# Performance work log

Hardware: AMD Instinct MI355X
Metric: run time of the kernel (lower is better)

## Reference

```python
import jax, jax.numpy as jnp
import numpy as np

B, S, D = 1, 4096, 1024
H = 16
HD = D // H  # 64
ROPE_THETA = 10000.0
NEG_INF = -1e9


def setup_inputs() -> dict:
    key = jax.random.key(0)
    ks = jax.random.split(key, 6)
    x = jax.random.normal(ks[0], (B, S, D), dtype=jnp.float32)
    # rotary frequencies: freqs_cis = exp(i * t * theta^{-2j/hd}), j in [0, hd/2)
    inv_freq = 1.0 / (ROPE_THETA ** (jnp.arange(0, HD, 2, dtype=jnp.float32) / HD))  # [HD/2]
    angles = jnp.arange(S, dtype=jnp.float32)[:, None] * inv_freq[None, :]  # [S, HD/2]
    freqs_cos = jnp.cos(angles)
    freqs_sin = jnp.sin(angles)
    # causal additive mask [S, S]
    mask = jnp.where(jnp.triu(jnp.ones((S, S), dtype=bool), k=1), NEG_INF, 0.0).astype(jnp.float32)
    scale = 0.02
    wq = jax.random.normal(ks[1], (D, D), dtype=jnp.float32) * scale
    wk = jax.random.normal(ks[2], (D, D), dtype=jnp.float32) * scale
    wv = jax.random.normal(ks[3], (D, D), dtype=jnp.float32) * scale
    wo = jax.random.normal(ks[4], (D, D), dtype=jnp.float32) * scale
    return {"x": x, "freqs_cos": freqs_cos, "freqs_sin": freqs_sin, "mask": mask,
            "wq": wq, "wk": wk, "wv": wv, "wo": wo}


def _apply_rope(t, cos, sin):
    # t: [B, S, H, HD]; cos/sin: [S, HD/2] -> broadcast [1, S, 1, HD/2]
    tr = t.reshape(*t.shape[:-1], HD // 2, 2)
    te, to = tr[..., 0], tr[..., 1]
    c = cos[None, :, None, :]
    s = sin[None, :, None, :]
    # complex multiply (te + i*to) * (c + i*s)
    oe = te * c - to * s
    oo = te * s + to * c
    return jnp.stack([oe, oo], axis=-1).reshape(t.shape)


def reference(x, freqs_cos, freqs_sin, mask, wq, wk, wv, wo):
    b, s, d = x.shape
    q = (x @ wq.T).reshape(b, s, H, HD)
    k = (x @ wk.T).reshape(b, s, H, HD)
    v = (x @ wv.T).reshape(b, s, H, HD)
    q = _apply_rope(q, freqs_cos, freqs_sin)
    k = _apply_rope(k, freqs_cos, freqs_sin)
    # [B, H, S, HD]
    q = q.transpose(0, 2, 1, 3)
    k = k.transpose(0, 2, 1, 3)
    v = v.transpose(0, 2, 1, 3)
    scores = jnp.einsum('bhqd,bhkd->bhqk', q, k) / jnp.sqrt(jnp.float32(HD))
    scores = scores + mask[None, None, :, :]
    probs = jax.nn.softmax(scores.astype(jnp.float32), axis=-1).astype(q.dtype)
    out = jnp.einsum('bhqk,bhkd->bhqd', probs, v)
    out = out.transpose(0, 2, 1, 3).reshape(b, s, d)
    return out @ wo.T
```

## Files before the change

### kernel.cpp

```cpp
#include <hip/hip_runtime.h>
#include <stdint.h>

typedef _Float16 f16;
typedef _Float16 v2h __attribute__((ext_vector_type(2)));
typedef _Float16 v4h __attribute__((ext_vector_type(4)));
typedef _Float16 v8h __attribute__((ext_vector_type(8)));
typedef float    v4f __attribute__((ext_vector_type(4)));

#define SEQ 4096
#define NH  16
#define DM  1024
#define QSCALE 0.18033688011112042f
#define MBASE 8.0f

__device__ __forceinline__ float exp2_(float x) {
#if __has_builtin(__builtin_amdgcn_exp2f)
  return __builtin_amdgcn_exp2f(x);
#else
  return exp2f(x);
#endif
}

__device__ __forceinline__ void gload_lds16(const void* g, void* l) {
  __builtin_amdgcn_global_load_lds((const __attribute__((address_space(1))) void*)g,
                                   (__attribute__((address_space(3))) void*)l,
                                   16, 0, 0);
}

#define NX 4194304
#define NW 1048576
__global__ void convert_kernel(const float* __restrict__ x,
                               const float* __restrict__ wq, const float* __restrict__ wk,
                               const float* __restrict__ wv, const float* __restrict__ wo,
                               f16* __restrict__ xf, f16* __restrict__ W, f16* __restrict__ Wo) {
  size_t e = ((size_t)blockIdx.x * 256 + threadIdx.x) * 4;
  const float* src; f16* dst;
  if (e < (size_t)NX) { src = x + e; dst = xf + e; }
  else {
    size_t j = e - NX; int wi = (int)(j >> 20); size_t off = j & (NW - 1);
    src = (wi == 0 ? wq : wi == 1 ? wk : wi == 2 ? wv : wo) + off;
    dst = (wi < 3 ? W + (size_t)wi * NW : Wo) + off;
  }
  v4f v = *(const v4f*)src;
  v4h o = { (f16)v.x, (f16)v.y, (f16)v.z, (f16)v.w };
  *(v4h*)dst = o;
}

template <typename OUTT>
__global__ __launch_bounds__(256, 2) void gemm_bt_f16(const f16* __restrict__ A,
                                                      const f16* __restrict__ B,
                                                      OUTT* __restrict__ C,
                                                      int M, int N, int K) {
  __shared__ __align__(16) f16 As[128 * 64];
  __shared__ __align__(16) f16 Bs[128 * 64];
  const int t = threadIdx.x;
  const int w = t >> 6, l = t & 63, quad = l >> 4, l15 = l & 15;
  const int wm = w & 1, wn = w >> 1;
  const int m0 = blockIdx.y * 128, n0 = blockIdx.x * 128;

  v4f acc[4][4];
#pragma unroll
  for (int i = 0; i < 4; ++i)
#pragma unroll
    for (int j = 0; j < 4; ++j) acc[i][j] = v4f{0.f, 0.f, 0.f, 0.f};

  const int nkt = K >> 6;
  for (int kt = 0; kt < nkt; ++kt) {
    __syncthreads();
#pragma unroll
    for (int i = 0; i < 4; ++i) {
      int c = i * 256 + t; int r = c >> 3, cc = c & 7; int sc = cc ^ (r & 7);
      gload_lds16(A + (size_t)(m0 + r) * K + kt * 64 + sc * 8, As + c * 8);
      gload_lds16(B + (size_t)(n0 + r) * K + kt * 64 + sc * 8, Bs + c * 8);
    }
    __syncthreads();
#pragma unroll
    for (int ks = 0; ks < 2; ++ks) {
      v8h af[4], bf[4];
#pragma unroll
      for (int i = 0; i < 4; ++i) {
        int ra = wm * 64 + i * 16 + l15;
        af[i] = *(const v8h*)(As + ra * 64 + (((ks * 4 + quad) ^ (ra & 7)) * 8));
        int rb = wn * 64 + i * 16 + l15;
        bf[i] = *(const v8h*)(Bs + rb * 64 + (((ks * 4 + quad) ^ (rb & 7)) * 8));
      }
#pragma unroll
      for (int i = 0; i < 4; ++i)
#pragma unroll
        for (int j = 0; j < 4; ++j)
          acc[i][j] = __builtin_amdgcn_mfma_f32_16x16x32_f16(af[i], bf[j], acc[i][j], 0, 0, 0);
    }
  }
#pragma unroll
  for (int i = 0; i < 4; ++i) {
    int m = m0 + wm * 64 + i * 16 + quad * 4;
#pragma unroll
    for (int j = 0; j < 4; ++j) {
      int n = n0 + wn * 64 + j * 16 + l15;
#pragma unroll
      for (int rg = 0; rg < 4; ++rg)
        C[(size_t)(m + rg) * N + n] = (OUTT)acc[i][j][rg];
    }
  }
}

__global__ void rope_kernel(const f16* __restrict__ qkv, const float* __restrict__ fc,
                            const float* __restrict__ fs, f16* __restrict__ Qh,
                            f16* __restrict__ Kh) {
  int idx = blockIdx.x * 256 + threadIdx.x;
  int s = idx >> 9, r = idx & 511, h = r >> 5, i = r & 31;
  size_t base = (size_t)s * 3072 + h * 64 + 2 * i;
  float qe = (float)qkv[base], qo = (float)qkv[base + 1];
  float ke = (float)qkv[base + 1024], ko = (float)qkv[base + 1025];
  float c = fc[s * 32 + i], sn = fs[s * 32 + i];
  size_t ob = ((size_t)(h * 4096 + s)) * 64 + 2 * i;
  v2h qo2 = { (f16)((qe * c - qo * sn) * QSCALE), (f16)((qe * sn + qo * c) * QSCALE) };
  v2h ko2 = { (f16)(ke * c - ko * sn), (f16)(ke * sn + ko * c) };
  *(v2h*)(Qh + ob) = qo2;
  *(v2h*)(Kh + ob) = ko2;
}

__global__ void vtrans_kernel(const f16* __restrict__ qkv, f16* __restrict__ Vt) {
  __shared__ __align__(16) f16 T[64][72];
  int h = blockIdx.x >> 6, sb = blockIdx.x & 63;
  int t = threadIdx.x, s0 = sb * 64;
#pragma unroll
  for (int i = 0; i < 2; ++i) {
    int r = i * 32 + (t >> 3), c8 = t & 7;
    *(v8h*)(&T[r][c8 * 8]) = *(const v8h*)(qkv + (size_t)(s0 + r) * 3072 + 2048 + h * 64 + c8 * 8);
  }
  __syncthreads();
#pragma unroll
  for (int i = 0; i < 4; ++i) {
    int idx = i * 256 + t;
    int d = idx >> 4;
    int sq = (idx & 15) * 4;
    int g = sq >> 5;
    int s32 = sq & 31;
    int kap = ((s32 >> 2) & 3) * 8 + (s32 >> 4) * 4;
    v4h o = { T[sq + 0][d], T[sq + 1][d], T[sq + 2][d], T[sq + 3][d] };
    *(v4h*)(Vt + (size_t)(h * 64 + d) * 4096 + s0 + g * 32 + kap) = o;
  }
}

__global__ __launch_bounds__(256, 4) void flash_kernel(const f16* __restrict__ Qh,
                                                       const f16* __restrict__ Kh,
                                                       const f16* __restrict__ Vt,
                                                       f16* __restrict__ Opart,
                                                       float* __restrict__ Lpart) {
  __shared__ __align__(16) f16 SM[16384];
  f16* Ks = SM;
  f16* Vs = SM + 8192;
  const int h = blockIdx.y;
  const int sr = 79 - (int)blockIdx.x;
  int qb, sp, nsp;
  if (sr < 8)       { qb = sr; sp = 0; nsp = 1; }
  else if (sr < 24) { int j = sr - 8;  qb = 8  + (j >> 1); sp = j & 1; nsp = 2; }
  else if (sr < 48) { int j = sr - 24; int q3 = j / 3; qb = 16 + q3; sp = j - 3 * q3; nsp = 3; }
  else              { int j = sr - 48; qb = 24 + (j >> 2); sp = j & 3; nsp = 4; }
  const int S = 2 * qb + 2;
  const int lo = (sp * S) / nsp, hi = ((sp + 1) * S) / nsp - 1;

  const int t = threadIdx.x, w = t >> 6, l = t & 63, quad = l >> 4, l15 = l & 15;
  const int q0w = qb * 128 + w * 32;

  v8h qf[2][2];
#pragma unroll
  for (int qt = 0; qt < 2; ++qt)
#pragma unroll
    for (int ks = 0; ks < 2; ++ks)
      qf[qt][ks] = *(const v8h*)(Qh + ((size_t)(h * 4096 + q0w + qt * 16 + l15)) * 64 + ks * 32 + quad * 8);

  v4f av[2][4];
#pragma unroll
  for (int qt = 0; qt < 2; ++qt)
#pragma unroll
    for (int db = 0; db < 4; ++db) av[qt][db] = v4f{0.f, 0.f, 0.f, 0.f};
  float lrun[2] = { 0.f, 0.f };

  const int c0 = t, c1 = 256 + t;
  const int r0 = c0 >> 3, sc0 = (c0 & 7) ^ (r0 & 7);
  const int r1 = c1 >> 3, sc1 = (c1 & 7) ^ (r1 & 7);
  const f16* KhB = Kh + (size_t)h * 4096 * 64;
  const f16* VtB = Vt + (size_t)h * 64 * 4096;

  {
    int koff = lo * 64;
    f16* Kd = Ks + (lo & 1) * 4096;
    f16* Vd = Vs + (lo & 1) * 4096;
    gload_lds16(KhB + (size_t)(koff + r0) * 64 + sc0 * 8, Kd + c0 * 8);
    gload_lds16(KhB + (size_t)(koff + r1) * 64 + sc1 * 8, Kd + c1 * 8);
    gload_lds16(VtB + (size_t)r0 * 4096 + koff + sc0 * 8, Vd + c0 * 8);
    gload_lds16(VtB + (size_t)r1 * 4096 + koff + sc1 * 8, Vd + c1 * 8);
  }

  for (int kb = lo; kb <= hi; ++kb) {
    __syncthreads();
    if (kb < hi) {
      int nb = (kb + 1) & 1;
      int koff = (kb + 1) * 64;
      gload_lds16(KhB + (size_t)(koff + r0) * 64 + sc0 * 8, Ks + nb * 4096 + c0 * 8);
      gload_lds16(KhB + (size_t)(koff + r1) * 64 + sc1 * 8, Ks + nb * 4096 + c1 * 8);
      gload_lds16(VtB + (size_t)r0 * 4096 + koff + sc0 * 8, Vs + nb * 4096 + c0 * 8);
      gload_lds16(VtB + (size_t)r1 * 4096 + koff + sc1 * 8, Vs + nb * 4096 + c1 * 8);
    }
    if (kb * 64 > q0w + 31) continue;
    const f16* Kc = Ks + (kb & 1) * 4096;
    const f16* Vc = Vs + (kb & 1) * 4096;

    v8h kf[4][2];
#pragma unroll
    for (int kt = 0; kt < 4; ++kt)
#pragma unroll
      for (int ks = 0; ks < 2; ++ks) {
        int r = kt * 16 + l15;
        kf[kt][ks] = *(const v8h*)(Kc + r * 64 + (((ks * 4 + quad) ^ (r & 7)) * 8));
      }

#pragma unroll
    for (int qt = 0; qt < 2; ++qt) {
      int qtb = q0w + qt * 16;
      if (kb * 64 > qtb + 15) continue;
      v4f st[4];
#pragma unroll
      for (int kt = 0; kt < 4; ++kt) {
        v4f z = v4f{ -MBASE, -MBASE, -MBASE, -MBASE };
        z = __builtin_amdgcn_mfma_f32_16x16x32_f16(kf[kt][0], qf[qt][0], z, 0, 0, 0);
        st[kt] = __builtin_amdgcn_mfma_f32_16x16x32_f16(kf[kt][1], qf[qt][1], z, 0, 0, 0);
      }
      if (kb * 64 + 63 > qtb) {
        int qg = qtb + l15;
#pragma unroll
        for (int kt = 0; kt < 4; ++kt)
#pragma unroll
          for (int jj = 0; jj < 4; ++jj) {
            int kg = kb * 64 + kt * 16 + quad * 4 + jj;
            if (kg > qg) st[kt][jj] = -1e30f;
          }
      }
      v4h pf[4];
      float rs = 0.f;
#pragma unroll
      for (int kt = 0; kt < 4; ++kt)
#pragma unroll
        for (int jj = 0; jj < 4; ++jj) {
          float p = exp2_(st[kt][jj]);
          rs += p;
          pf[kt][jj] = (f16)p;
        }
      lrun[qt] += rs;
      v8h pg[2];
#pragma unroll
      for (int g = 0; g < 2; ++g) {
        pg[g][0] = pf[2 * g][0]; pg[g][1] = pf[2 * g][1];
        pg[g][2] = pf[2 * g][2]; pg[g][3] = pf[2 * g][3];
        pg[g][4] = pf[2 * g + 1][0]; pg[g][5] = pf[2 * g + 1][1];
        pg[g][6] = pf[2 * g + 1][2]; pg[g][7] = pf[2 * g + 1][3];
      }
#pragma unroll
      for (int db = 0; db < 4; ++db) {
        int r = db * 16 + l15;
#pragma unroll
        for (int g = 0; g < 2; ++g) {
          v8h vf = *(const v8h*)(Vc + r * 64 + (((g * 4 + quad) ^ (r & 7)) * 8));
          av[qt][db] = __builtin_amdgcn_mfma_f32_16x16x32_f16(vf, pg[g], av[qt][db], 0, 0, 0);
        }
      }
    }
  }
  const size_t base = (size_t)(h * 80 + sr);
#pragma unroll
  for (int qt = 0; qt < 2; ++qt) {
    float lr = lrun[qt];
    lr += __shfl_xor(lr, 16);
    lr += __shfl_xor(lr, 32);
    int q = w * 32 + qt * 16 + l15;
    if (quad == 0) Lpart[base * 128 + q] = lr;
#pragma unroll
    for (int db = 0; db < 4; ++db) {
      v4h o = { (f16)av[qt][db][0], (f16)av[qt][db][1],
                (f16)av[qt][db][2], (f16)av[qt][db][3] };
      *(v4h*)(Opart + base * 8192 + (size_t)q * 64 + db * 16 + quad * 4) = o;
    }
  }
}

__global__ void combine_kernel(const f16* __restrict__ Opart, const float* __restrict__ Lpart,
                               f16* __restrict__ attn) {
  int qb = blockIdx.x, h = blockIdx.y;
  int nsp, base;
  if (qb < 8)       { nsp = 1; base = qb; }
  else if (qb < 16) { nsp = 2; base = 8 + 2 * (qb - 8); }
  else if (qb < 24) { nsp = 3; base = 24 + 3 * (qb - 16); }
  else              { nsp = 4; base = 48 + 4 * (qb - 24); }
  int t = threadIdx.x, q = t >> 1, dh = (t & 1) * 32;
  float l = 0.f;
  float o[32];
#pragma unroll
  for (int c = 0; c < 32; ++c) o[c] = 0.f;
  for (int s = 0; s < nsp; ++s) {
    size_t sb = (size_t)(h * 80 + base + s);
    const f16* P = Opart + sb * 8192 + q * 64 + dh;
#pragma unroll
    for (int c = 0; c < 4; ++c) {
      v8h v = *(const v8h*)(P + c * 8);
#pragma unroll
      for (int j = 0; j < 8; ++j) o[c * 8 + j] += (float)v[j];
    }
    l += Lpart[sb * 128 + q];
  }
  float inv = 1.f / l;
#pragma unroll
  for (int c = 0; c < 4; ++c) {
    v8h v;
#pragma unroll
    for (int j = 0; j < 8; ++j) v[j] = (f16)(o[c * 8 + j] * inv);
    *(v8h*)(attn + (size_t)(qb * 128 + q) * 1024 + h * 64 + dh + c * 8) = v;
  }
}

extern "C" void kernel_launch(void* const* d_in, const int* in_sizes, int n_in,
                              void* d_out, int out_size, void* d_ws, size_t ws_size,
                              hipStream_t stream) {
  (void)in_sizes; (void)n_in; (void)out_size; (void)ws_size;
  const float* x  = (const float*)d_in[0];
  const float* fc = (const float*)d_in[1];
  const float* fs = (const float*)d_in[2];
  const float* wq = (const float*)d_in[4];
  const float* wk = (const float*)d_in[5];
  const float* wv = (const float*)d_in[6];
  const float* wo = (const float*)d_in[7];
  float* out = (float*)d_out;
  char* ws = (char*)d_ws;

  f16* xf    = (f16*)(ws);
  f16* W     = (f16*)(ws + 8388608);
  f16* Wo    = (f16*)(ws + 14680064);
  f16* QKV   = (f16*)(ws + 16777216);
  f16* Qh    = (f16*)(ws + 41943040);
  f16* Kh    = (f16*)(ws + 50331648);
  f16* Vt    = (f16*)(ws + 58720256);
  f16* attn  = xf;
  f16* Opart = QKV;
  float* Lpart = (float*)(ws + 16777216 + 20971520);

  convert_kernel<<<dim3(8192), dim3(256), 0, stream>>>(x, wq, wk, wv, wo, xf, W, Wo);
  gemm_bt_f16<f16><<<dim3(24, 32), dim3(256), 0, stream>>>(xf, W, QKV, 4096, 3072, 1024);
  rope_kernel<<<dim3(8192), dim3(256), 0, stream>>>(QKV, fc, fs, Qh, Kh);
  vtrans_kernel<<<dim3(1024), dim3(256), 0, stream>>>(QKV, Vt);
  flash_kernel<<<dim3(80, 16), dim3(256), 0, stream>>>(Qh, Kh, Vt, Opart, Lpart);
  combine_kernel<<<dim3(32, 16), dim3(256), 0, stream>>>(Opart, Lpart, attn);
  gemm_bt_f16<float><<<dim3(8, 32), dim3(256), 0, stream>>>(attn, Wo, out, 4096, 1024, 1024);
}
```

Measured before the change: 258.5 us.

## Fuse RoPE into QKV GEMM epilogue, retile output GEMM, reorder flash grid

Applies RoPE and the Q scaling directly in the QKV GEMM epilogue. It uses a lane shuffle to fetch the paired even/odd element and writes Q and K straight into the head-major layout, which removes the separate rope kernel and the round trip of Q and K through global memory. V is written to a smaller temporary buffer before the transpose. The output projection gets its own kernel with 128x64 tiles and a 3-block occupancy hint, which doubles the block count for better CU fill. The flash grid is flattened so heads vary fastest, and the P fragment packing is simplified. In exchange, the epilogue stores are scattered 2-byte writes with extra fc/fs loads per element.

```diff
diff --git a/kernel.cpp b/kernel.cpp
--- a/kernel.cpp
+++ b/kernel.cpp
@@ -46,17 +46,21 @@
   *(v4h*)dst = o;
 }
 
-template <typename OUTT>
-__global__ __launch_bounds__(256, 2) void gemm_bt_f16(const f16* __restrict__ A,
-                                                      const f16* __restrict__ B,
-                                                      OUTT* __restrict__ C,
-                                                      int M, int N, int K) {
+__global__ __launch_bounds__(256, 2) void gemm_qkv_kernel(const f16* __restrict__ A,
+                                                          const f16* __restrict__ B,
+                                                          const float* __restrict__ fc,
+                                                          const float* __restrict__ fs,
+                                                          f16* __restrict__ Qh,
+                                                          f16* __restrict__ Kh,
+                                                          f16* __restrict__ Vtmp) {
+  const int K = 1024;
   __shared__ __align__(16) f16 As[128 * 64];
   __shared__ __align__(16) f16 Bs[128 * 64];
   const int t = threadIdx.x;
   const int w = t >> 6, l = t & 63, quad = l >> 4, l15 = l & 15;
   const int wm = w & 1, wn = w >> 1;
-  const int m0 = blockIdx.y * 128, n0 = blockIdx.x * 128;
+  const int bx = blockIdx.x;
+  const int m0 = blockIdx.y * 128, n0 = bx * 128;
 
   v4f acc[4][4];
 #pragma unroll
@@ -64,8 +68,7 @@
 #pragma unroll
     for (int j = 0; j < 4; ++j) acc[i][j] = v4f{0.f, 0.f, 0.f, 0.f};
 
-  const int nkt = K >> 6;
-  for (int kt = 0; kt < nkt; ++kt) {
+  for (int kt = 0; kt < 16; ++kt) {
     __syncthreads();
 #pragma unroll
     for (int i = 0; i < 4; ++i) {
@@ -91,43 +94,52 @@
           acc[i][j] = __builtin_amdgcn_mfma_f32_16x16x32_f16(af[i], bf[j], acc[i][j], 0, 0, 0);
     }
   }
-#pragma unroll
-  for (int i = 0; i < 4; ++i) {
-    int m = m0 + wm * 64 + i * 16 + quad * 4;
+  const int mat = bx >> 3;
+  if (mat < 2) {
+    f16* dst = (mat == 0) ? Qh : Kh;
+    const int hh = (bx & 7) * 2 + wn;
 #pragma unroll
     for (int j = 0; j < 4; ++j) {
-      int n = n0 + wn * 64 + j * 16 + l15;
-#pragma unroll
-      for (int rg = 0; rg < 4; ++rg)
-        C[(size_t)(m + rg) * N + n] = (OUTT)acc[i][j][rg];
-    }
-  }
-}
-
-__global__ void rope_kernel(const f16* __restrict__ qkv, const float* __restrict__ fc,
-                            const float* __restrict__ fs, f16* __restrict__ Qh,
-                            f16* __restrict__ Kh) {
-  int idx = blockIdx.x * 256 + threadIdx.x;
-  int s = idx >> 9, r = idx & 511, h = r >> 5, i = r & 31;
-  size_t base = (size_t)s * 3072 + h * 64 + 2 * i;
-  float qe = (float)qkv[base], qo = (float)qkv[base + 1];
-  float ke = (float)qkv[base + 1024], ko = (float)qkv[base + 1025];
-  float c = fc[s * 32 + i], sn = fs[s * 32 + i];
-  size_t ob = ((size_t)(h * 4096 + s)) * 64 + 2 * i;
-  v2h qo2 = { (f16)((qe * c - qo * sn) * QSCALE), (f16)((qe * sn + qo * c) * QSCALE) };
-  v2h ko2 = { (f16)(ke * c - ko * sn), (f16)(ke * sn + ko * c) };
-  *(v2h*)(Qh + ob) = qo2;
-  *(v2h*)(Kh + ob) = ko2;
-}
-
-__global__ void vtrans_kernel(const f16* __restrict__ qkv, f16* __restrict__ Vt) {
+      const int d = j * 16 + l15;
+      const int i2 = d >> 1;
+      const float sgnmul = (l15 & 1) ? 1.f : -1.f;
+#pragma unroll
+      for (int i = 0; i < 4; ++i) {
+#pragma unroll
+        for (int rg = 0; rg < 4; ++rg) {
+          float own = acc[i][j][rg];
+          float par = __shfl_xor(own, 1);
+          int m = m0 + wm * 64 + i * 16 + quad * 4 + rg;
+          float c = fc[m * 32 + i2], sn = fs[m * 32 + i2];
+          if (mat == 0) { c *= QSCALE; sn *= QSCALE; }
+          float out = own * c + par * (sn * sgnmul);
+          dst[((size_t)(hh * 4096 + m)) * 64 + d] = (f16)out;
+        }
+      }
+    }
+  } else {
+#pragma unroll
+    for (int i = 0; i < 4; ++i) {
+      int m = m0 + wm * 64 + i * 16 + quad * 4;
+#pragma unroll
+      for (int j = 0; j < 4; ++j) {
+        int nf = (bx - 16) * 128 + wn * 64 + j * 16 + l15;
+#pragma unroll
+        for (int rg = 0; rg < 4; ++rg)
+          Vtmp[(size_t)(m + rg) * 1024 + nf] = (f16)acc[i][j][rg];
+      }
+    }
+  }
+}
+
+__global__ void vtrans_kernel(const f16* __restrict__ Vtmp, f16* __restrict__ Vt) {
   __shared__ __align__(16) f16 T[64][72];
   int h = blockIdx.x >> 6, sb = blockIdx.x & 63;
   int t = threadIdx.x, s0 = sb * 64;
 #pragma unroll
   for (int i = 0; i < 2; ++i) {
     int r = i * 32 + (t >> 3), c8 = t & 7;
-    *(v8h*)(&T[r][c8 * 8]) = *(const v8h*)(qkv + (size_t)(s0 + r) * 3072 + 2048 + h * 64 + c8 * 8);
+    *(v8h*)(&T[r][c8 * 8]) = *(const v8h*)(Vtmp + (size_t)(s0 + r) * 1024 + h * 64 + c8 * 8);
   }
   __syncthreads();
 #pragma unroll
@@ -151,8 +163,8 @@
   __shared__ __align__(16) f16 SM[16384];
   f16* Ks = SM;
   f16* Vs = SM + 8192;
-  const int h = blockIdx.y;
-  const int sr = 79 - (int)blockIdx.x;
+  const int h = blockIdx.x & 15;
+  const int sr = 79 - ((int)blockIdx.x >> 4);
   int qb, sp, nsp;
   if (sr < 8)       { qb = sr; sp = 0; nsp = 1; }
   else if (sr < 24) { int j = sr - 8;  qb = 8  + (j >> 1); sp = j & 1; nsp = 2; }
@@ -238,7 +250,7 @@
             if (kg > qg) st[kt][jj] = -1e30f;
           }
       }
-      v4h pf[4];
+      v8h pg[2];
       float rs = 0.f;
 #pragma unroll
       for (int kt = 0; kt < 4; ++kt)
@@ -246,17 +258,9 @@
         for (int jj = 0; jj < 4; ++jj) {
           float p = exp2_(st[kt][jj]);
           rs += p;
-          pf[kt][jj] = (f16)p;
+          pg[kt >> 1][(kt & 1) * 4 + jj] = (f16)p;
         }
       lrun[qt] += rs;
-      v8h pg[2];
-#pragma unroll
-      for (int g = 0; g < 2; ++g) {
-        pg[g][0] = pf[2 * g][0]; pg[g][1] = pf[2 * g][1];
-        pg[g][2] = pf[2 * g][2]; pg[g][3] = pf[2 * g][3];
-        pg[g][4] = pf[2 * g + 1][0]; pg[g][5] = pf[2 * g + 1][1];
-        pg[g][6] = pf[2 * g + 1][2]; pg[g][7] = pf[2 * g + 1][3];
-      }
 #pragma unroll
       for (int db = 0; db < 4; ++db) {
         int r = db * 16 + l15;
@@ -316,6 +320,69 @@
 #pragma unroll
     for (int j = 0; j < 8; ++j) v[j] = (f16)(o[c * 8 + j] * inv);
     *(v8h*)(attn + (size_t)(qb * 128 + q) * 1024 + h * 64 + dh + c * 8) = v;
+  }
+}
+
+__global__ __launch_bounds__(256, 3) void gemm_out_kernel(const f16* __restrict__ A,
+                                                          const f16* __restrict__ B,
+                                                          float* __restrict__ C) {
+  const int K = 1024, N = 1024;
+  __shared__ __align__(16) f16 As[128 * 64];
+  __shared__ __align__(16) f16 Bs[64 * 64];
+  const int t = threadIdx.x;
+  const int w = t >> 6, l = t & 63, quad = l >> 4, l15 = l & 15;
+  const int wm = w & 1, wn = w >> 1;
+  const int m0 = blockIdx.y * 128, n0 = blockIdx.x * 64;
+
+  v4f acc[4][2];
+#pragma unroll
+  for (int i = 0; i < 4; ++i)
+#pragma unroll
+    for (int j = 0; j < 2; ++j) acc[i][j] = v4f{0.f, 0.f, 0.f, 0.f};
+
+  for (int kt = 0; kt < 16; ++kt) {
+    __syncthreads();
+#pragma unroll
+    for (int i = 0; i < 4; ++i) {
+      int c = i * 256 + t; int r = c >> 3, cc = c & 7; int sc = cc ^ (r & 7);
+      gload_lds16(A + (size_t)(m0 + r) * K + kt * 64 + sc * 8, As + c * 8);
+    }
+#pragma unroll
+    for (int i = 0; i < 2; ++i) {
+      int c = i * 256 + t; int r = c >> 3, cc = c & 7; int sc = cc ^ (r & 7);
+      gload_lds16(B + (size_t)(n0 + r) * K + kt * 64 + sc * 8, Bs + c * 8);
+    }
+    __syncthreads();
+#pragma unroll
+    for (int ks = 0; ks < 2; ++ks) {
+      v8h af[4], bf[2];
+#pragma unroll
+      for (int i = 0; i < 4; ++i) {
+        int ra = wm * 64 + i * 16 + l15;
+        af[i] = *(const v8h*)(As + ra * 64 + (((ks * 4 + quad) ^ (ra & 7)) * 8));
+      }
+#pragma unroll
+      for (int j = 0; j < 2; ++j) {
+        int rb = wn * 32 + j * 16 + l15;
+        bf[j] = *(const v8h*)(Bs + rb * 64 + (((ks * 4 + quad) ^ (rb & 7)) * 8));
+      }
+#pragma unroll
+      for (int i = 0; i < 4; ++i)
+#pragma unroll
+        for (int j = 0; j < 2; ++j)
+          acc[i][j] = __builtin_amdgcn_mfma_f32_16x16x32_f16(af[i], bf[j], acc[i][j], 0, 0, 0);
+    }
+  }
+#pragma unroll
+  for (int i = 0; i < 4; ++i) {
+    int m = m0 + wm * 64 + i * 16 + quad * 4;
+#pragma unroll
+    for (int j = 0; j < 2; ++j) {
+      int n = n0 + wn * 32 + j * 16 + l15;
+#pragma unroll
+      for (int rg = 0; rg < 4; ++rg)
+        C[(size_t)(m + rg) * N + n] = acc[i][j][rg];
+    }
   }
 }
 
@@ -336,19 +403,18 @@
   f16* xf    = (f16*)(ws);
   f16* W     = (f16*)(ws + 8388608);
   f16* Wo    = (f16*)(ws + 14680064);
-  f16* QKV   = (f16*)(ws + 16777216);
+  f16* Vtmp  = (f16*)(ws + 16777216);
   f16* Qh    = (f16*)(ws + 41943040);
   f16* Kh    = (f16*)(ws + 50331648);
   f16* Vt    = (f16*)(ws + 58720256);
   f16* attn  = xf;
-  f16* Opart = QKV;
+  f16* Opart = Vtmp;
   float* Lpart = (float*)(ws + 16777216 + 20971520);
 
   convert_kernel<<<dim3(8192), dim3(256), 0, stream>>>(x, wq, wk, wv, wo, xf, W, Wo);
-  gemm_bt_f16<f16><<<dim3(24, 32), dim3(256), 0, stream>>>(xf, W, QKV, 4096, 3072, 1024);
-  rope_kernel<<<dim3(8192), dim3(256), 0, stream>>>(QKV, fc, fs, Qh, Kh);
-  vtrans_kernel<<<dim3(1024), dim3(256), 0, stream>>>(QKV, Vt);
-  flash_kernel<<<dim3(80, 16), dim3(256), 0, stream>>>(Qh, Kh, Vt, Opart, Lpart);
+  gemm_qkv_kernel<<<dim3(24, 32), dim3(256), 0, stream>>>(xf, W, fc, fs, Qh, Kh, Vtmp);
+  vtrans_kernel<<<dim3(1024), dim3(256), 0, stream>>>(Vtmp, Vt);
+  flash_kernel<<<dim3(1280), dim3(256), 0, stream>>>(Qh, Kh, Vt, Opart, Lpart);
   combine_kernel<<<dim3(32, 16), dim3(256), 0, stream>>>(Opart, Lpart, attn);
-  gemm_bt_f16<float><<<dim3(8, 32), dim3(256), 0, stream>>>(attn, Wo, out, 4096, 1024, 1024);
-}
+  gemm_out_kernel<<<dim3(16, 32), dim3(256), 0, stream>>>(attn, Wo, out);
+}
```

New measurement: 243.4 us. -5.9%, faster.
